# Performance work log

Measured on AMD Instinct MI355X. Metric: run time of the kernel, lower is better.

The kernel has to match this reference:

```python
import jax, jax.numpy as jnp
import numpy as np

M = 64    # multiplicity (channels per harmonic degree)
P = 64    # positional encoding dim
EPS = 1e-5


def sinusoidal_pe(N, P):
    pos = jnp.arange(N, dtype=jnp.float32)[:, None]
    div = jnp.exp(jnp.arange(0, P, 2, dtype=jnp.float32) * (-np.log(10000.0) / P))
    pe = jnp.zeros((N, P), dtype=jnp.float32)
    pe = pe.at[:, 0::2].set(jnp.sin(pos * div))
    pe = pe.at[:, 1::2].set(jnp.cos(pos * div))
    return pe


def split_irreps(h):
    # h: [B, N, 4M] -> scalar part [B,N,M], vector part [B,N,M,3]
    B, N, _ = h.shape
    h4 = h.reshape(B, N, M, 4)
    return h4[..., 0], h4[..., 1:]


def merge_irreps(s, v):
    B, N, _ = s.shape
    return jnp.concatenate([s[..., None], v], axis=-1).reshape(B, N, M * 4)


def hyena_block(h, Wq, Wk, Wv, filt, Wo):
    # Hyena-style gated long convolution: q * conv(k * v), FFT circular conv along seq
    N = h.shape[1]
    q = h @ Wq
    k = h @ Wk
    v = h @ Wv
    kf = jnp.fft.rfft(filt, n=N, axis=0)                       # [N//2+1, H]
    conv = jnp.fft.irfft(jnp.fft.rfft(k * v, n=N, axis=1) * kf[None], n=N, axis=1)
    return (q * conv) @ Wo


def reg_linear(h, W0, W1):
    # degree-wise linear mixing across multiplicity (equivariant)
    s, v = split_irreps(h)
    return merge_irreps(jnp.einsum('bnm,mk->bnk', s, W0),
                        jnp.einsum('bnmd,mk->bnkd', v, W1))


def reg_batchnorm(h, g0, g1):
    # normalize per-channel irrep norms over (batch, tokens); learnable per-channel gain
    s, v = split_irreps(h)
    n0 = jnp.sqrt(jnp.mean(s * s, axis=(0, 1)) + EPS)          # [M]
    n1 = jnp.sqrt(jnp.mean(jnp.sum(v * v, axis=-1), axis=(0, 1)) + EPS)
    return merge_irreps(s / n0 * g0, v / n1[:, None] * g1[:, None])


def norm_activation(h):
    # norm-gated nonlinearity: each irrep scaled by sigmoid of its norm (equivariant)
    s, v = split_irreps(h)
    vn = jnp.sqrt(jnp.sum(v * v, axis=-1, keepdims=True) + EPS)
    return merge_irreps(s * jax.nn.sigmoid(jnp.abs(s)), v * jax.nn.sigmoid(vn))


def setup_inputs() -> dict:
    key = jax.random.key(0)
    B, N = 64, 1024
    D = M * 4
    H = [360, 360, 160]   # 10*sum(2l+1,l<=5)=360, 360, 10*sum(2l+1,l<=3)=160
    ks = iter(jax.random.split(key, 64))
    def rn(shape, scale=0.02):
        return jax.random.normal(next(ks), shape, dtype=jnp.float32) * scale
    inp = {
        'x': jax.random.normal(next(ks), (B, N, 3), dtype=jnp.float32),
        'tok_emb': rn((3, P)),
        'Wf': rn((P, M)),
        'wv': rn((M,), 0.5),
        'w_out': rn((M,), 0.5),
    }
    for i, Hi in enumerate(H, start=1):
        inp[f'Wq{i}'] = rn((D, Hi)); inp[f'Wk{i}'] = rn((D, Hi)); inp[f'Wv{i}'] = rn((D, Hi))
        inp[f'filt{i}'] = rn((N, Hi)); inp[f'Wo{i}'] = rn((Hi, D))
        inp[f'Wm0_{i}'] = rn((M, M)); inp[f'Wm1_{i}'] = rn((M, M))
        inp[f'g0_{i}'] = jnp.ones((M,), jnp.float32); inp[f'g1_{i}'] = jnp.ones((M,), jnp.float32)
    return inp


def reference(x, tok_emb, Wf, wv, w_out,
              Wq1, Wk1, Wv1, filt1, Wo1, Wm0_1, Wm1_1, g0_1, g1_1,
              Wq2, Wk2, Wv2, filt2, Wo2, Wm0_2, Wm1_2, g0_2, g1_2,
              Wq3, Wk3, Wv3, filt3, Wo3, Wm0_3, Wm1_3, g0_3, g1_3):
    B, N, _ = x.shape
    # invariant features: sinusoidal PE + token-type embedding (alternating 0/1, last token 2)
    pe = sinusoidal_pe(N, P)
    tt = jnp.arange(N) % 2
    tt = tt.at[-1].set(2)
    f = pe + tok_emb[tt]                                        # [N, P]
    # input conversion: invariants -> degree-0 channels; input vector -> degree-1 channels
    s0 = jnp.broadcast_to((f @ Wf)[None], (B, N, M))
    v0 = x[:, :, None, :] * wv[None, None, :, None]             # [B, N, M, 3]
    h = merge_irreps(s0, v0)                                    # [B, N, 4M]
    layers = [
        (Wq1, Wk1, Wv1, filt1, Wo1, Wm0_1, Wm1_1, g0_1, g1_1),
        (Wq2, Wk2, Wv2, filt2, Wo2, Wm0_2, Wm1_2, g0_2, g1_2),
        (Wq3, Wk3, Wv3, filt3, Wo3, Wm0_3, Wm1_3, g0_3, g1_3),
    ]
    for (Wq, Wk, Wv_, filt, Wo, Wm0, Wm1, g0, g1) in layers:
        h = h + hyena_block(h, Wq, Wk, Wv_, filt, Wo)           # hyena + residual
        y = reg_linear(h, Wm0, Wm1)                             # mlp
        y = reg_batchnorm(y, g0, g1)                            # batch norm
        y = norm_activation(y)                                  # norm activation
        h = h + y                                               # residual
    pooled = h.mean(axis=1)                                     # [B, 4M] mean pool over tokens
    _, vpool = split_irreps(pooled[:, None, :])                 # [B, 1, M, 3]
    return jnp.einsum('bmd,m->bd', vpool[:, 0], w_out)          # [B, 3]
```

## Files before the change

### kernel.cpp

```cpp
#include <hip/hip_runtime.h>
#include <math.h>

namespace {

typedef __bf16 bf16_t;
typedef bf16_t bf16x8 __attribute__((ext_vector_type(8)));
typedef float floatx4 __attribute__((ext_vector_type(4)));

constexpr int kN = 1024;
constexpr int kM = 64;
constexpr int kP = 64;
constexpr float kEps = 1e-5f;
constexpr int kFN = 1024;
constexpr size_t kYOFF = 16777216;

__device__ __forceinline__ float sigmoidf(float v) { return 1.0f / (1.0f + expf(-v)); }

__device__ __forceinline__ floatx4 mfma16(bf16x8 a, bf16x8 b, floatx4 c) {
  return __builtin_amdgcn_mfma_f32_16x16x32_bf16(a, b, c, 0, 0, 0);
}

__device__ __forceinline__ void fma3(floatx4& acc, bf16x8 ah, bf16x8 al,
                                     bf16x8 bh, bf16x8 bl) {
  acc = mfma16(ah, bh, acc);
  acc = mfma16(ah, bl, acc);
  acc = mfma16(al, bh, acc);
}

__device__ __forceinline__ void fma2(floatx4& acc, bf16x8 ah, bf16x8 bh, bf16x8 bl) {
  acc = mfma16(ah, bh, acc);
  acc = mfma16(ah, bl, acc);
}

union U4 { uint4 u; bf16_t b[8]; };
union Pk4 { uint2 u; bf16_t b[4]; };
union Ub2 { uint u; bf16_t b[2]; };

__device__ __forceinline__ void glds16(const bf16_t* g, bf16_t* l) {
  __builtin_amdgcn_global_load_lds(
      (const __attribute__((address_space(1))) void*)g,
      (__attribute__((address_space(3))) void*)l, 16, 0, 0);
}

__device__ __forceinline__ size_t hidx(int r, int d8) {
  const int rb = r >> 6, rr = r & 63;
  return (size_t)(rb * 8 + (d8 >> 2)) * 4096 + (rr >> 4) * 1024 + (d8 & 3) * 128 + (rr & 15) * 8;
}

__device__ __forceinline__ int zi(int i) { return i + (i >> 4); }

__device__ __forceinline__ float2 cadd(float2 a, float2 b) { return {a.x + b.x, a.y + b.y}; }
__device__ __forceinline__ float2 csub(float2 a, float2 b) { return {a.x - b.x, a.y - b.y}; }
__device__ __forceinline__ float2 cmul(float2 a, float2 w) {
  return {a.x * w.x - a.y * w.y, a.x * w.y + a.y * w.x};
}
__device__ __forceinline__ float2 cmulc(float2 a, float2 w) {
  return {a.x * w.x + a.y * w.y, a.y * w.x - a.x * w.y};
}

__global__ void k_s0(const float* __restrict__ tok_emb, const float* __restrict__ Wf,
                     float* __restrict__ s0) {
  __shared__ float f[kP];
  const int n = blockIdx.x;
  const int t = threadIdx.x;
  const int tt = (n == kN - 1) ? 2 : (n & 1);
  const int j = t >> 1;
  const float cexp = (float)(-9.210340371976184 / 64.0);
  const float divj = expf((float)(2 * j) * cexp);
  const float ang = (float)n * divj;
  const float pe = (t & 1) ? cosf(ang) : sinf(ang);
  f[t] = pe + tok_emb[tt * kP + t];
  __syncthreads();
  float acc = 0.0f;
#pragma unroll 8
  for (int p = 0; p < kP; ++p) acc = fmaf(f[p], Wf[p * kM + t], acc);
  s0[n * kM + t] = acc;
}

__global__ void k_h0(const float* __restrict__ x, const float* __restrict__ wv,
                     const float* __restrict__ s0, bf16_t* __restrict__ hsh) {
  const int idx = blockIdx.x * 256 + threadIdx.x;
  const int r = idx >> 5, d8 = idx & 31;
  const int n = r & (kN - 1);
  const int m0 = d8 * 2, m1 = m0 + 1;
  const float w0 = wv[m0], w1 = wv[m1];
  const float x0 = x[r * 3 + 0], x1 = x[r * 3 + 1], x2 = x[r * 3 + 2];
  float f[8];
  f[0] = s0[n * kM + m0]; f[1] = x0 * w0; f[2] = x1 * w0; f[3] = x2 * w0;
  f[4] = s0[n * kM + m1]; f[5] = x0 * w1; f[6] = x1 * w1; f[7] = x2 * w1;
  U4 oh, ol;
#pragma unroll
  for (int i = 0; i < 8; ++i) {
    const bf16_t h_ = (bf16_t)f[i];
    oh.b[i] = h_; ol.b[i] = (bf16_t)(f[i] - (float)h_);
  }
  const size_t base = hidx(r, d8);
  *(uint4*)(hsh + base) = oh.u;
  *(uint4*)(hsh + base + 512) = ol.u;
}

__global__ void k_wqkv3(const float* __restrict__ Wq0, const float* __restrict__ Wk0,
                        const float* __restrict__ Wv0,
                        const float* __restrict__ Wq1, const float* __restrict__ Wk1,
                        const float* __restrict__ Wv1,
                        const float* __restrict__ Wq2, const float* __restrict__ Wk2,
                        const float* __restrict__ Wv2, bf16_t* __restrict__ wall3) {
  const int l = blockIdx.y;
  const int H = (l == 2) ? 160 : 360;
  const int gy = (l == 2) ? 3 : 6;
  const int c = blockIdx.x;
  if (c >= gy * 64) return;
  const int k = threadIdx.x;
  const float* Wq = (l == 0) ? Wq0 : ((l == 1) ? Wq1 : Wq2);
  const float* Wk = (l == 0) ? Wk0 : ((l == 1) ? Wk1 : Wk2);
  const float* Wv = (l == 0) ? Wv0 : ((l == 1) ? Wv1 : Wv2);
  bf16_t* wall = wall3 + ((l == 2) ? 1179648 : (size_t)l * 589824);
  const bool ok = c < H;
  const float w[3] = {ok ? Wq[k * H + c] : 0.f, ok ? Wk[k * H + c] : 0.f,
                      ok ? Wv[k * H + c] : 0.f};
  const int ct = c >> 6, cgrp = (c >> 4) & 3, cl = c & 15;
  const int kc = k >> 5, quad = (k >> 3) & 3, off = k & 7;
  const size_t base = (size_t)(ct * 8 + kc) * 12288 + cgrp * 512 + quad * 128 + cl * 8 + off;
#pragma unroll
  for (int mat = 0; mat < 3; ++mat) {
    const bf16_t hi = (bf16_t)w[mat];
    wall[base + mat * 4096] = hi;
    wall[base + mat * 4096 + 2048] = (bf16_t)(w[mat] - (float)hi);
  }
}

__global__ void k_wo3(const float* __restrict__ Wo0, const float* __restrict__ Wo1,
                      const float* __restrict__ Wo2, bf16_t* __restrict__ WoF3) {
  const int l = blockIdx.y;
  const int H = (l == 2) ? 160 : 360;
  const float* Wo = (l == 0) ? Wo0 : ((l == 1) ? Wo1 : Wo2);
  bf16_t* WoF = WoF3 + (size_t)l * 196608;
  const int d = blockIdx.x;
  const int c = threadIdx.x;
  const float w = (c < H) ? Wo[c * 256 + d] : 0.f;
  const int dt = d >> 6, dgrp = (d >> 4) & 3, dl = d & 15;
  const int kc = c >> 5, quad = (c >> 3) & 3, off = c & 7;
  const size_t base = (size_t)(dt * 12 + kc) * 4096 + dgrp * 512 + quad * 128 + dl * 8 + off;
  const bf16_t hi = (bf16_t)w;
  WoF[base] = hi;
  WoF[base + 2048] = (bf16_t)(w - (float)hi);
}

__global__ void k_bt3(const float* __restrict__ W00, const float* __restrict__ W10,
                      const float* __restrict__ W01, const float* __restrict__ W11,
                      const float* __restrict__ W02, const float* __restrict__ W12,
                      bf16_t* __restrict__ BtF3) {
  const int l = blockIdx.y;
  const float* W0 = (l == 0) ? W00 : ((l == 1) ? W01 : W02);
  const float* W1 = (l == 0) ? W10 : ((l == 1) ? W11 : W12);
  bf16_t* BtF = BtF3 + (size_t)l * 131072;
  const int col = blockIdx.x, row = threadIdx.x;
  const int k = col >> 2, ck = col & 3, m = row >> 2, cm = row & 3;
  float v = 0.f;
  if (cm == ck) v = (ck == 0 ? W0 : W1)[m * 64 + k];
  const int ct = col >> 6, cgrp = (col >> 4) & 3, cl = col & 15;
  const int kc = row >> 5, quad = (row >> 3) & 3, off = row & 7;
  const size_t base = (size_t)(ct * 8 + kc) * 4096 + cgrp * 512 + quad * 128 + cl * 8 + off;
  const bf16_t hi = (bf16_t)v;
  BtF[base] = hi;
  BtF[base + 2048] = (bf16_t)(v - (float)hi);
}

__global__ void k_tw(float2* __restrict__ twg) {
  const int j = blockIdx.x * 256 + threadIdx.x;
  if (j < kFN / 2) {
    float s, c;
    sincosf(-6.283185307179586f * (float)j / (float)kFN, &s, &c);
    twg[j].x = c; twg[j].y = s;
  }
}

__device__ __forceinline__ void dif_step(float2* z, const float2* tw, int m, int p) {
  const int pm = p & (m - 1);
  const int j = ((p & ~(m - 1)) << 2) | pm;
  const int tm2 = 512 / (2 * m), tm1 = 512 / m;
  const float2 x0 = z[zi(j)], x1 = z[zi(j + m)];
  const float2 x2 = z[zi(j + 2 * m)], x3 = z[zi(j + 3 * m)];
  const float2 w2 = tw[pm * tm2], w2b = tw[(pm + m) * tm2], w1 = tw[pm * tm1];
  const float2 a0 = cadd(x0, x2), a2 = cmul(csub(x0, x2), w2);
  const float2 a1 = cadd(x1, x3), a3 = cmul(csub(x1, x3), w2b);
  z[zi(j)]         = cadd(a0, a1);
  z[zi(j + m)]     = cmul(csub(a0, a1), w1);
  z[zi(j + 2 * m)] = cadd(a2, a3);
  z[zi(j + 3 * m)] = cmul(csub(a2, a3), w1);
}

__device__ __forceinline__ void dit_step(float2* z, const float2* tw, int m, int p) {
  const int pm = p & (m - 1);
  const int j = ((p & ~(m - 1)) << 2) | pm;
  const int tm2 = 512 / (2 * m), tm1 = 512 / m;
  const float2 x0 = z[zi(j)], x1 = z[zi(j + m)];
  const float2 x2 = z[zi(j + 2 * m)], x3 = z[zi(j + 3 * m)];
  const float2 w1 = tw[pm * tm1], w2 = tw[pm * tm2], w2b = tw[(pm + m) * tm2];
  const float2 c1 = cmulc(x1, w1), c3 = cmulc(x3, w1);
  const float2 b0 = cadd(x0, c1), b1 = csub(x0, c1);
  const float2 b2 = cadd(x2, c3), b3 = csub(x2, c3);
  const float2 d2 = cmulc(b2, w2), d3 = cmulc(b3, w2b);
  z[zi(j)]         = cadd(b0, d2);
  z[zi(j + 2 * m)] = csub(b0, d2);
  z[zi(j + m)]     = cadd(b1, d3);
  z[zi(j + 3 * m)] = csub(b1, d3);
}

__device__ void fft_dif(float2* z, const float2* tw) {
  const int p = threadIdx.x;
#pragma unroll
  for (int m = 256; m >= 1; m >>= 2) {
    __syncthreads();
    dif_step(z, tw, m, p);
  }
}

__device__ void fft_dif2_hi(float2* za, float2* zb, const float2* tw) {
  const int p = threadIdx.x;
#pragma unroll
  for (int m = 64; m >= 4; m >>= 2) {
    __syncthreads();
    dif_step(za, tw, m, p);
    dif_step(zb, tw, m, p);
  }
}

__device__ void fft_dit_inv2_hi(float2* za, float2* zb, const float2* tw) {
  const int p = threadIdx.x;
#pragma unroll
  for (int m = 4; m <= 256; m <<= 2) {
    __syncthreads();
    dit_step(za, tw, m, p);
    dit_step(zb, tw, m, p);
  }
}

__global__ __launch_bounds__(256) void k_kf3(const float* __restrict__ f0,
    const float* __restrict__ f1, const float* __restrict__ f2,
    const float2* __restrict__ twg, float2* __restrict__ kf3) {
  __shared__ float2 z[kFN + kFN / 16];
  __shared__ float2 tw[kFN / 2];
  const int bid = blockIdx.x;
  const int l = (bid < 360) ? 0 : ((bid < 720) ? 1 : 2);
  const int c = bid - ((l == 0) ? 0 : ((l == 1) ? 360 : 720));
  const int H = (l == 2) ? 160 : 360;
  const float* filt = (l == 0) ? f0 : ((l == 1) ? f1 : f2);
  float2* kf = kf3 + (size_t)l * 368640;
  for (int j = threadIdx.x; j < kFN / 2; j += 256) tw[j] = twg[j];
  for (int n = threadIdx.x; n < kFN; n += 256) {
    z[zi(n)].x = filt[n * H + c];
    z[zi(n)].y = 0.0f;
  }
  fft_dif(z, tw);
  __syncthreads();
  for (int j = threadIdx.x; j < kFN; j += 256) kf[c * kFN + j] = z[zi(j)];
}

__global__ __launch_bounds__(256) void k_conv(const bf16_t* __restrict__ kvb,
    const bf16_t* __restrict__ qb, bf16_t* __restrict__ prodb,
    const float2* __restrict__ kf, const float2* __restrict__ twg, int H) {
  __shared__ float2 za[kFN + kFN / 16];
  __shared__ float2 zb[kFN + kFN / 16];
  __shared__ float2 tw[kFN / 2];
  const int blk = blockIdx.x;
  const int c = blk % H;
  const int pb = blk / H;
  const size_t off0 = ((size_t)((4 * pb) * H + c)) << 10;
  const size_t off1 = ((size_t)((4 * pb + 1) * H + c)) << 10;
  const size_t off2 = ((size_t)((4 * pb + 2) * H + c)) << 10;
  const size_t off3 = ((size_t)((4 * pb + 3) * H + c)) << 10;
  for (int j = threadIdx.x; j < kFN / 2; j += 256) tw[j] = twg[j];
  {
    const int p = threadIdx.x;
    float2 xa[4], xb[4];
#pragma unroll
    for (int e = 0; e < 4; ++e) {
      const int idx = p + e * 256;
      xa[e].x = (float)kvb[off0 + idx]; xa[e].y = (float)kvb[off1 + idx];
      xb[e].x = (float)kvb[off2 + idx]; xb[e].y = (float)kvb[off3 + idx];
    }
    const float2 w2 = twg[p], w2b = twg[p + 256], w1 = twg[2 * p];
#pragma unroll
    for (int arr = 0; arr < 2; ++arr) {
      float2* z = arr ? zb : za;
      const float2* x = arr ? xb : xa;
      const float2 a0 = cadd(x[0], x[2]), a2 = cmul(csub(x[0], x[2]), w2);
      const float2 a1 = cadd(x[1], x[3]), a3 = cmul(csub(x[1], x[3]), w2b);
      z[zi(p)]       = cadd(a0, a1);
      z[zi(p + 256)] = cmul(csub(a0, a1), w1);
      z[zi(p + 512)] = cadd(a2, a3);
      z[zi(p + 768)] = cmul(csub(a2, a3), w1);
    }
  }
  fft_dif2_hi(za, zb, tw);
  __syncthreads();
  {
    const int p = threadIdx.x;
    const float2 B0 = kf[c * kFN + 4 * p + 0];
    const float2 B1 = kf[c * kFN + 4 * p + 1];
    const float2 B2 = kf[c * kFN + 4 * p + 2];
    const float2 B3 = kf[c * kFN + 4 * p + 3];
#pragma unroll
    for (int arr = 0; arr < 2; ++arr) {
      float2* z = arr ? zb : za;
      const float2 x0 = z[zi(4 * p)], x1 = z[zi(4 * p + 1)];
      const float2 x2 = z[zi(4 * p + 2)], x3 = z[zi(4 * p + 3)];
      const float2 a0 = cadd(x0, x2), a2 = csub(x0, x2);
      const float2 a1 = cadd(x1, x3), dd = csub(x1, x3);
      const float2 a3 = {dd.y, -dd.x};
      const float2 y0 = cadd(a0, a1), y1 = csub(a0, a1);
      const float2 y2 = cadd(a2, a3), y3 = csub(a2, a3);
      const float2 o0 = cmul(y0, B0), o1 = cmul(y1, B1);
      const float2 o2 = cmul(y2, B2), o3 = cmul(y3, B3);
      const float2 t0 = cadd(o0, o1), t1 = csub(o0, o1);
      const float2 t2 = cadd(o2, o3), t3 = csub(o2, o3);
      const float2 d3 = {-t3.y, t3.x};
      z[zi(4 * p)]     = cadd(t0, t2);
      z[zi(4 * p + 2)] = csub(t0, t2);
      z[zi(4 * p + 1)] = cadd(t1, d3);
      z[zi(4 * p + 3)] = csub(t1, d3);
    }
  }
  fft_dit_inv2_hi(za, zb, tw);
  __syncthreads();
  const float s = 1.0f / (float)kFN;
  for (int n2 = threadIdx.x; n2 < 512; n2 += 256) {
    Ub2 q0, q1, q2, q3, o0, o1, o2, o3;
    q0.u = *(const uint*)(qb + off0 + 2 * n2);
    q1.u = *(const uint*)(qb + off1 + 2 * n2);
    q2.u = *(const uint*)(qb + off2 + 2 * n2);
    q3.u = *(const uint*)(qb + off3 + 2 * n2);
    o0.b[0] = (bf16_t)((za[zi(2 * n2)].x * s) * (float)q0.b[0]);
    o0.b[1] = (bf16_t)((za[zi(2 * n2 + 1)].x * s) * (float)q0.b[1]);
    o1.b[0] = (bf16_t)((za[zi(2 * n2)].y * s) * (float)q1.b[0]);
    o1.b[1] = (bf16_t)((za[zi(2 * n2 + 1)].y * s) * (float)q1.b[1]);
    o2.b[0] = (bf16_t)((zb[zi(2 * n2)].x * s) * (float)q2.b[0]);
    o2.b[1] = (bf16_t)((zb[zi(2 * n2 + 1)].x * s) * (float)q2.b[1]);
    o3.b[0] = (bf16_t)((zb[zi(2 * n2)].y * s) * (float)q3.b[0]);
    o3.b[1] = (bf16_t)((zb[zi(2 * n2 + 1)].y * s) * (float)q3.b[1]);
    *(uint*)(prodb + off0 + 2 * n2) = o0.u;
    *(uint*)(prodb + off1 + 2 * n2) = o1.u;
    *(uint*)(prodb + off2 + 2 * n2) = o2.u;
    *(uint*)(prodb + off3 + 2 * n2) = o3.u;
  }
}

__global__ __launch_bounds__(256) void k_qkv(const bf16_t* __restrict__ hsh,
    const bf16_t* __restrict__ wall, int H,
    bf16_t* __restrict__ qtb, bf16_t* __restrict__ kvb) {
  __shared__ bf16_t lds[20480];
  const int gy = (H + 63) >> 6;
  const int bid = blockIdx.x;
  const int xcd = bid & 7, sseq = bid >> 3;
  const int ct = sseq % gy;
  const int rb2 = (sseq / gy) * 8 + xcd;
  const int rb0 = rb2 * 2, rb1 = rb0 + 1;
  const int t = threadIdx.x;
  const int lane = t & 63, wave = t >> 6;
  const int l15 = lane & 15, quad = lane >> 4;
  const int c0 = ct * 64;
  const int wr = (wave & 1) * 32, wc = (wave >> 1) * 32;
  const int wr16 = (wave & 1) * 2, wc16 = (wave >> 1) * 2;
  const int q128l = quad * 128 + l15 * 8;
  floatx4 aq[2][2][2] = {}, ak_[2][2][2] = {}, av_[2][2][2] = {};
  for (int kt = 0; kt < 8; ++kt) {
    {
      const bf16_t* A0 = hsh + (size_t)(rb0 * 8 + kt) * 4096;
      const bf16_t* A1 = hsh + (size_t)(rb1 * 8 + kt) * 4096;
      const bf16_t* Bs = wall + (size_t)(ct * 8 + kt) * 12288;
#pragma unroll
      for (int s = 0; s < 10; ++s) {
        const int seg = wave * 10 + s;
        const bf16_t* src = (seg < 8) ? (A0 + seg * 512)
                          : (seg < 16) ? (A1 + (seg - 8) * 512)
                                       : (Bs + (seg - 16) * 512);
        glds16(src + lane * 8, &lds[seg * 512]);
      }
    }
    __syncthreads();
    bf16x8 ah[2][2], al[2][2];
#pragma unroll
    for (int rbx = 0; rbx < 2; ++rbx)
#pragma unroll
      for (int i = 0; i < 2; ++i) {
        ah[rbx][i] = *(const bf16x8*)(lds + rbx * 4096 + ((wr16 + i) * 2 + 0) * 512 + q128l);
        al[rbx][i] = *(const bf16x8*)(lds + rbx * 4096 + ((wr16 + i) * 2 + 1) * 512 + q128l);
      }
#pragma unroll
    for (int mat = 0; mat < 3; ++mat) {
      const int bb = 8192 + mat * 4096;
#pragma unroll
      for (int j = 0; j < 2; ++j) {
        const bf16x8 bh = *(const bf16x8*)(lds + bb + (wc16 + j) * 512 + q128l);
        const bf16x8 bl = *(const bf16x8*)(lds + bb + 2048 + (wc16 + j) * 512 + q128l);
#pragma unroll
        for (int rbx = 0; rbx < 2; ++rbx)
#pragma unroll
          for (int i = 0; i < 2; ++i) {
            floatx4& a = (mat == 0) ? aq[rbx][i][j]
                       : (mat == 1) ? ak_[rbx][i][j] : av_[rbx][i][j];
            fma3(a, ah[rbx][i], al[rbx][i], bh, bl);
          }
      }
    }
    __syncthreads();
  }
#pragma unroll
  for (int rbx = 0; rbx < 2; ++rbx) {
    const int r0 = (rb0 + rbx) * 64;
    const int b = r0 >> 10;
    const int n0 = r0 & 1023;
#pragma unroll
    for (int j = 0; j < 2; ++j) {
      const int c = c0 + wc + j * 16 + l15;
      if (c < H) {
        const size_t rbw = (((size_t)(b * H + c)) << 10) + n0 + wr + quad * 4;
#pragma unroll
        for (int i = 0; i < 2; ++i) {
          Pk4 pq, pk;
#pragma unroll
          for (int r = 0; r < 4; ++r) {
            pq.b[r] = (bf16_t)aq[rbx][i][j][r];
            pk.b[r] = (bf16_t)(ak_[rbx][i][j][r] * av_[rbx][i][j][r]);
          }
          *(uint2*)(qtb + rbw + i * 16) = pq.u;
          *(uint2*)(kvb + rbw + i * 16) = pk.u;
        }
      }
    }
  }
}

__global__ __launch_bounds__(256) void k_mix(const bf16_t* __restrict__ pv, int H, int KT,
    const bf16_t* __restrict__ WoF, bf16_t* __restrict__ hsh) {
  __shared__ float smem[4352];
  bf16_t* lsm = (bf16_t*)smem;
  const int r0 = blockIdx.x * 64;
  const int t = threadIdx.x;
  const int lane = t & 63, wave = t >> 6;
  const int l15 = lane & 15, quad = lane >> 4;
  const int b = r0 >> 10, n0 = r0 & 1023;
  const int wr = (wave & 1) * 32, wh = wave >> 1;
  const int q128l = quad * 128 + l15 * 8;
  floatx4 acc[2][8] = {};
  const int cl = t >> 3, n8 = (t & 7) * 8;
  {
    U4 val;
    val.u = make_uint4(0, 0, 0, 0);
    if (cl < H)
      val.u = *(const uint4*)(pv + ((((size_t)(b * H + cl)) << 10) + n0 + n8));
#pragma unroll
    for (int u = 0; u < 8; ++u) lsm[(n8 + u) * 40 + cl] = val.b[u];
  }
  for (int kt = 0; kt < KT; ++kt) {
    const int cur = kt & 1;
    const bool have = (kt + 1 < KT);
    U4 nxt;
    nxt.u = make_uint4(0, 0, 0, 0);
    if (have) {
      const int c = (kt + 1) * 32 + cl;
      if (c < H)
        nxt.u = *(const uint4*)(pv + ((((size_t)(b * H + c)) << 10) + n0 + n8));
    }
    __syncthreads();
    const bf16_t* Ls = lsm + cur * 2560;
    const bf16x8 ah0 = *(const bf16x8*)(Ls + (wr + l15) * 40 + quad * 8);
    const bf16x8 ah1 = *(const bf16x8*)(Ls + (wr + 16 + l15) * 40 + quad * 8);
#pragma unroll
    for (int j = 0; j < 8; ++j) {
      const int jj = wh * 8 + j;
      const int dt = jj >> 2, dgrp = jj & 3;
      const bf16_t* Bb = WoF + (size_t)(dt * 12 + kt) * 4096 + dgrp * 512 + q128l;
      const bf16x8 bh = *(const bf16x8*)Bb;
      const bf16x8 bl = *(const bf16x8*)(Bb + 2048);
      fma2(acc[0][j], ah0, bh, bl);
      fma2(acc[1][j], ah1, bh, bl);
    }
    if (have) {
      bf16_t* Ld = lsm + (cur ^ 1) * 2560;
#pragma unroll
      for (int u = 0; u < 8; ++u) Ld[(n8 + u) * 40 + cl] = nxt.b[u];
    }
  }
  const int nl = t >> 2, q4 = t & 3;
  const int r = r0 + nl;
#pragma unroll
  for (int g = 0; g < 4; ++g) {
    __syncthreads();
    if (wh == (g >> 1)) {
#pragma unroll
      for (int jl = 0; jl < 4; ++jl) {
        const int j = (g & 1) * 4 + jl;
#pragma unroll
        for (int i = 0; i < 2; ++i)
#pragma unroll
          for (int rr = 0; rr < 4; ++rr)
            smem[(wr + i * 16 + quad * 4 + rr) * 68 + jl * 16 + l15] = acc[i][j][rr];
      }
    }
    __syncthreads();
#pragma unroll
    for (int u8 = 0; u8 < 2; ++u8) {
      const int d8 = g * 8 + q4 * 2 + u8;
      const size_t base = hidx(r, d8);
      U4 hi, lo;
      hi.u = *(const uint4*)(hsh + base);
      lo.u = *(const uint4*)(hsh + base + 512);
      U4 oh, ol;
#pragma unroll
      for (int i = 0; i < 8; ++i) {
        const float f = (float)hi.b[i] + (float)lo.b[i] +
                        smem[nl * 68 + (q4 * 2 + u8) * 8 + i];
        const bf16_t h_ = (bf16_t)f;
        oh.b[i] = h_; ol.b[i] = (bf16_t)(f - (float)h_);
      }
      *(uint4*)(hsh + base) = oh.u;
      *(uint4*)(hsh + base + 512) = ol.u;
    }
  }
}

__global__ __launch_bounds__(256) void k_reg(const bf16_t* __restrict__ hsh,
    const bf16_t* __restrict__ BtF,
    bf16_t* __restrict__ ybf, float* __restrict__ partial) {
  __shared__ float smf[12288];
  __shared__ float red[256];
  bf16_t* lds = (bf16_t*)smf;
  const int bid = blockIdx.x;
  const int xcd = bid & 7, sseq = bid >> 3;
  const int ct = sseq & 3;
  const int rb2 = (sseq >> 2) * 8 + xcd;
  const int rb0 = rb2 * 2, rb1 = rb0 + 1;
  const int t = threadIdx.x;
  const int lane = t & 63, wave = t >> 6;
  const int l15 = lane & 15, quad = lane >> 4;
  const int c0 = ct * 64;
  const int wr = (wave & 1) * 32, wc = (wave >> 1) * 32;
  const int wr16 = (wave & 1) * 2, wc16 = (wave >> 1) * 2;
  const int q128l = quad * 128 + l15 * 8;
  floatx4 acc[2][2][2] = {};
  auto stage = [&](int kt, int buf) {
    const bf16_t* A0 = hsh + (size_t)(rb0 * 8 + kt) * 4096;
    const bf16_t* A1 = hsh + (size_t)(rb1 * 8 + kt) * 4096;
    const bf16_t* Bs = BtF + (size_t)(ct * 8 + kt) * 4096;
#pragma unroll
    for (int s = 0; s < 6; ++s) {
      const int seg = wave * 6 + s;
      const bf16_t* src = (seg < 8) ? (A0 + seg * 512)
                        : (seg < 16) ? (A1 + (seg - 8) * 512)
                                     : (Bs + (seg - 16) * 512);
      glds16(src + lane * 8, &lds[buf * 12288 + seg * 512]);
    }
  };
  stage(0, 0);
  __syncthreads();
  for (int kt = 0; kt < 8; ++kt) {
    const int cur = kt & 1;
    if (kt < 7) stage(kt + 1, cur ^ 1);
    const bf16_t* Lb = lds + cur * 12288;
    bf16x8 ah[2][2], al[2][2];
#pragma unroll
    for (int rbx = 0; rbx < 2; ++rbx)
#pragma unroll
      for (int i = 0; i < 2; ++i) {
        ah[rbx][i] = *(const bf16x8*)(Lb + rbx * 4096 + ((wr16 + i) * 2 + 0) * 512 + q128l);
        al[rbx][i] = *(const bf16x8*)(Lb + rbx * 4096 + ((wr16 + i) * 2 + 1) * 512 + q128l);
      }
#pragma unroll
    for (int j = 0; j < 2; ++j) {
      const bf16x8 bh = *(const bf16x8*)(Lb + 8192 + (wc16 + j) * 512 + q128l);
      const bf16x8 bl = *(const bf16x8*)(Lb + 8192 + 2048 + (wc16 + j) * 512 + q128l);
#pragma unroll
      for (int rbx = 0; rbx < 2; ++rbx)
#pragma unroll
        for (int i = 0; i < 2; ++i)
          fma3(acc[rbx][i][j], ah[rbx][i], al[rbx][i], bh, bl);
    }
    __syncthreads();
  }
#pragma unroll
  for (int rbx = 0; rbx < 2; ++rbx)
#pragma unroll
    for (int j = 0; j < 2; ++j) {
      float s = 0.f;
#pragma unroll
      for (int i = 0; i < 2; ++i)
#pragma unroll
        for (int r = 0; r < 4; ++r)
          s = fmaf(acc[rbx][i][j][r], acc[rbx][i][j][r], s);
      s += __shfl_down(s, 32);
      s += __shfl_down(s, 16);
      if (lane < 16) red[rbx * 128 + wave * 32 + j * 16 + lane] = s;
    }
#pragma unroll
  for (int rbx = 0; rbx < 2; ++rbx) {
    __syncthreads();
#pragma unroll
    for (int i = 0; i < 2; ++i)
#pragma unroll
      for (int j = 0; j < 2; ++j)
#pragma unroll
        for (int r = 0; r < 4; ++r)
          smf[(wr + i * 16 + quad * 4 + r) * 68 + wc + j * 16 + l15] = acc[rbx][i][j][r];
    __syncthreads();
    const int nl = t >> 2, q4 = t & 3;
    const int r0 = (rb0 + rbx) * 64;
    const size_t gi = (size_t)(r0 + nl) * 256 + c0 + q4 * 16;
#pragma unroll
    for (int u2 = 0; u2 < 2; ++u2) {
      U4 oh, ol;
#pragma unroll
      for (int i = 0; i < 8; ++i) {
        const float f = smf[nl * 68 + q4 * 16 + u2 * 8 + i];
        const bf16_t h_ = (bf16_t)f;
        oh.b[i] = h_; ol.b[i] = (bf16_t)(f - (float)h_);
      }
      *(uint4*)(ybf + gi + u2 * 8) = oh.u;
      *(uint4*)(ybf + kYOFF + gi + u2 * 8) = ol.u;
    }
  }
  if (t < 64) {
    const int w0 = (t >= 32) ? 2 : 0;
    const float v0 = red[w0 * 32 + (t & 31)] + red[(w0 + 1) * 32 + (t & 31)];
    const float v1 = red[128 + w0 * 32 + (t & 31)] + red[128 + (w0 + 1) * 32 + (t & 31)];
    partial[(size_t)rb0 * 256 + c0 + t] = v0;
    partial[(size_t)rb1 * 256 + c0 + t] = v1;
  }
}

__global__ __launch_bounds__(256) void k_stat(const float* __restrict__ partial,
                                              float* __restrict__ st) {
  __shared__ float sm1[16][16];
  __shared__ float tot[16];
  const int bb = blockIdx.x;
  const int t = threadIdx.x;
  const int col16 = t & 15, rgrp = t >> 4;
  const int c = bb * 16 + col16;
  float s = 0.f;
  for (int r = rgrp; r < 1024; r += 16) s += partial[(size_t)r * 256 + c];
  sm1[rgrp][col16] = s;
  __syncthreads();
  if (t < 16) {
    float v = 0.f;
#pragma unroll
    for (int g = 0; g < 16; ++g) v += sm1[g][t];
    tot[t] = v;
  }
  __syncthreads();
  if (t < 4) {
    const int m = bb * 4 + t;
    st[m] = tot[4 * t];
    st[64 + m] = tot[4 * t + 1] + tot[4 * t + 2] + tot[4 * t + 3];
  }
}

__global__ void k_bnact(const bf16_t* __restrict__ ybf, const float* __restrict__ stats,
    const float* __restrict__ g0, const float* __restrict__ g1, bf16_t* __restrict__ hsh) {
  const int idx = blockIdx.x * 256 + threadIdx.x;
  const int r = idx >> 5, d8 = idx & 31;
  const int m0 = d8 * 2, m1 = m0 + 1;
  const float i00 = g0[m0] / sqrtf(stats[m0] * (1.0f / 65536.0f) + kEps);
  const float i10 = g1[m0] / sqrtf(stats[64 + m0] * (1.0f / 65536.0f) + kEps);
  const float i01 = g0[m1] / sqrtf(stats[m1] * (1.0f / 65536.0f) + kEps);
  const float i11 = g1[m1] / sqrtf(stats[64 + m1] * (1.0f / 65536.0f) + kEps);
  const size_t ye = (size_t)r * 256 + d8 * 8;
  U4 yh, yl;
  yh.u = *(const uint4*)(ybf + ye);
  yl.u = *(const uint4*)(ybf + kYOFF + ye);
  float yv[8];
#pragma unroll
  for (int i = 0; i < 8; ++i) yv[i] = (float)yh.b[i] + (float)yl.b[i];
  float a[8];
  {
    const float s = yv[0] * i00;
    const float vx = yv[1] * i10, vy = yv[2] * i10, vz = yv[3] * i10;
    const float so = s * sigmoidf(fabsf(s));
    const float vn = sqrtf(fmaf(vx, vx, fmaf(vy, vy, vz * vz)) + kEps);
    const float gv = sigmoidf(vn);
    a[0] = so; a[1] = vx * gv; a[2] = vy * gv; a[3] = vz * gv;
  }
  {
    const float s = yv[4] * i01;
    const float vx = yv[5] * i11, vy = yv[6] * i11, vz = yv[7] * i11;
    const float so = s * sigmoidf(fabsf(s));
    const float vn = sqrtf(fmaf(vx, vx, fmaf(vy, vy, vz * vz)) + kEps);
    const float gv = sigmoidf(vn);
    a[4] = so; a[5] = vx * gv; a[6] = vy * gv; a[7] = vz * gv;
  }
  const size_t base = hidx(r, d8);
  U4 hi, lo;
  hi.u = *(const uint4*)(hsh + base);
  lo.u = *(const uint4*)(hsh + base + 512);
  U4 oh, ol;
#pragma unroll
  for (int i = 0; i < 8; ++i) {
    const float f = (float)hi.b[i] + (float)lo.b[i] + a[i];
    const bf16_t h_ = (bf16_t)f;
    oh.b[i] = h_; ol.b[i] = (bf16_t)(f - (float)h_);
  }
  *(uint4*)(hsh + base) = oh.u;
  *(uint4*)(hsh + base + 512) = ol.u;
}

__global__ __launch_bounds__(256) void k_bnpool(const bf16_t* __restrict__ ybf,
    const float* __restrict__ stats, const float* __restrict__ g0,
    const float* __restrict__ g1, const bf16_t* __restrict__ hsh,
    const float* __restrict__ w_out, float* __restrict__ pp) {
  __shared__ float r0s[256], r1s[256], r2s[256];
  const int t = threadIdx.x;
  const int idx = blockIdx.x * 256 + t;
  const int r = idx >> 5, d8 = idx & 31;
  const int m0 = d8 * 2, m1 = m0 + 1;
  const float i00 = g0[m0] / sqrtf(stats[m0] * (1.0f / 65536.0f) + kEps);
  const float i10 = g1[m0] / sqrtf(stats[64 + m0] * (1.0f / 65536.0f) + kEps);
  const float i01 = g0[m1] / sqrtf(stats[m1] * (1.0f / 65536.0f) + kEps);
  const float i11 = g1[m1] / sqrtf(stats[64 + m1] * (1.0f / 65536.0f) + kEps);
  const size_t ye = (size_t)r * 256 + d8 * 8;
  U4 yh, yl;
  yh.u = *(const uint4*)(ybf + ye);
  yl.u = *(const uint4*)(ybf + kYOFF + ye);
  float yv[8];
#pragma unroll
  for (int i = 0; i < 8; ++i) yv[i] = (float)yh.b[i] + (float)yl.b[i];
  float a[8];
  {
    const float s = yv[0] * i00;
    const float vx = yv[1] * i10, vy = yv[2] * i10, vz = yv[3] * i10;
    const float so = s * sigmoidf(fabsf(s));
    const float vn = sqrtf(fmaf(vx, vx, fmaf(vy, vy, vz * vz)) + kEps);
    const float gv = sigmoidf(vn);
    a[0] = so; a[1] = vx * gv; a[2] = vy * gv; a[3] = vz * gv;
  }
  {
    const float s = yv[4] * i01;
    const float vx = yv[5] * i11, vy = yv[6] * i11, vz = yv[7] * i11;
    const float so = s * sigmoidf(fabsf(s));
    const float vn = sqrtf(fmaf(vx, vx, fmaf(vy, vy, vz * vz)) + kEps);
    const float gv = sigmoidf(vn);
    a[4] = so; a[5] = vx * gv; a[6] = vy * gv; a[7] = vz * gv;
  }
  const size_t base = hidx(r, d8);
  U4 hi, lo;
  hi.u = *(const uint4*)(hsh + base);
  lo.u = *(const uint4*)(hsh + base + 512);
  float f[8];
#pragma unroll
  for (int i = 0; i < 8; ++i) f[i] = (float)hi.b[i] + (float)lo.b[i] + a[i];
  const float w0 = w_out[m0], w1 = w_out[m1];
  r0s[t] = f[1] * w0 + f[5] * w1;
  r1s[t] = f[2] * w0 + f[6] * w1;
  r2s[t] = f[3] * w0 + f[7] * w1;
  __syncthreads();
  for (int s = 128; s > 0; s >>= 1) {
    if (t < s) { r0s[t] += r0s[t + s]; r1s[t] += r1s[t + s]; r2s[t] += r2s[t + s]; }
    __syncthreads();
  }
  if (t == 0) {
    pp[blockIdx.x * 3 + 0] = r0s[0];
    pp[blockIdx.x * 3 + 1] = r1s[0];
    pp[blockIdx.x * 3 + 2] = r2s[0];
  }
}

__global__ void k_pool2(const float* __restrict__ pp, float* __restrict__ out) {
  const int t = threadIdx.x;
  const int b = t / 3, comp = t % 3;
  float s = 0.f;
  for (int k = 0; k < 128; ++k) s += pp[(size_t)(b * 128 + k) * 3 + comp];
  out[t] = s * (1.0f / kN);
}

}

extern "C" void kernel_launch(void* const* d_in, const int* in_sizes, int n_in,
                              void* d_out, int out_size, void* d_ws, size_t ws_size,
                              hipStream_t stream) {
  const float* x       = (const float*)d_in[0];
  const float* tok_emb = (const float*)d_in[1];
  const float* Wf      = (const float*)d_in[2];
  const float* wv      = (const float*)d_in[3];
  const float* w_out   = (const float*)d_in[4];

  float* ws    = (float*)d_ws;
  bf16_t* hsh  = (bf16_t*)ws;
  bf16_t* kvb  = (bf16_t*)(ws + 16777216);
  bf16_t* qtb  = (bf16_t*)(ws + 28573696);
  bf16_t* prodb = (bf16_t*)(ws + 40370176);
  bf16_t* ybf  = prodb;
  float*  partial = ws + 40370176 + 20000000;
  float*  s0   = ws + 40370176 + 23592960;
  float*  kf3  = s0 + 65536;
  bf16_t* wall3 = (bf16_t*)(kf3 + 1802240);
  bf16_t* WoF3  = wall3 + 1474560;
  bf16_t* BtF3  = WoF3 + 589824;
  float* stats = (float*)(BtF3 + 393216);
  float* twg   = stats + 384;

  k_tw<<<2, 256, 0, stream>>>((float2*)twg);
  k_s0<<<kN, 64, 0, stream>>>(tok_emb, Wf, s0);
  k_h0<<<8192, 256, 0, stream>>>(x, wv, s0, hsh);
  k_wqkv3<<<dim3(384, 3), 256, 0, stream>>>(
      (const float*)d_in[5], (const float*)d_in[6], (const float*)d_in[7],
      (const float*)d_in[14], (const float*)d_in[15], (const float*)d_in[16],
      (const float*)d_in[23], (const float*)d_in[24], (const float*)d_in[25], wall3);
  k_wo3<<<dim3(256, 3), 384, 0, stream>>>(
      (const float*)d_in[9], (const float*)d_in[18], (const float*)d_in[27], WoF3);
  k_bt3<<<dim3(256, 3), 256, 0, stream>>>(
      (const float*)d_in[10], (const float*)d_in[11],
      (const float*)d_in[19], (const float*)d_in[20],
      (const float*)d_in[28], (const float*)d_in[29], BtF3);
  k_kf3<<<880, 256, 0, stream>>>(
      (const float*)d_in[8], (const float*)d_in[17], (const float*)d_in[26],
      (const float2*)twg, (float2*)kf3);

  for (int l = 0; l < 3; ++l) {
    const float* g0   = (const float*)d_in[5 + 9 * l + 7];
    const float* g1   = (const float*)d_in[5 + 9 * l + 8];
    const int H = (l == 2) ? 160 : 360;
    const int gy = (H + 63) / 64;
    const int KT = gy * 2;
    bf16_t* wall = wall3 + ((l == 2) ? 1179648 : (size_t)l * 589824);
    bf16_t* WoF  = WoF3 + (size_t)l * 196608;
    bf16_t* BtF  = BtF3 + (size_t)l * 131072;
    const float2* kf = (const float2*)kf3 + (size_t)l * 368640;
    float* st = stats + l * 128;

    k_qkv<<<gy * 512, 256, 0, stream>>>(hsh, wall, H, qtb, kvb);
    k_conv<<<16 * H, 256, 0, stream>>>(kvb, qtb, prodb, kf, (const float2*)twg, H);
    k_mix<<<1024, 256, 0, stream>>>(prodb, H, KT, WoF, hsh);
    k_reg<<<2048, 256, 0, stream>>>(hsh, BtF, ybf, partial);
    k_stat<<<16, 256, 0, stream>>>(partial, st);
    if (l < 2) {
      k_bnact<<<8192, 256, 0, stream>>>(ybf, st, g0, g1, hsh);
    } else {
      k_bnpool<<<8192, 256, 0, stream>>>(ybf, st, g0, g1, hsh, w_out, partial);
    }
  }

  k_pool2<<<1, 192, 0, stream>>>(partial, (float*)d_out);
}
```

Measured before the change: 1.022 ms.

## Retile k_reg so each block computes all 256 output columns for one row block

The regular-linear GEMM kernel now gives each block one 64-row block and all 256 output columns instead of two row blocks by 64 columns. Activation tiles are loaded once per block rather than once per column tile, and the grid halves to 1024 blocks. Double buffering of the LDS staging is removed: each k-step loads then syncs, which may expose global-to-LDS latency. Each wave holds more accumulators (16 floatx4), raising register pressure and reducing parallelism per kernel.

```diff
diff --git a/kernel.cpp b/kernel.cpp
--- a/kernel.cpp
+++ b/kernel.cpp
@@ -524,89 +524,82 @@
 __global__ __launch_bounds__(256) void k_reg(const bf16_t* __restrict__ hsh,
     const bf16_t* __restrict__ BtF,
     bf16_t* __restrict__ ybf, float* __restrict__ partial) {
-  __shared__ float smf[12288];
-  __shared__ float red[256];
-  bf16_t* lds = (bf16_t*)smf;
+  __shared__ bf16_t lds[20480];
+  __shared__ float red[512];
+  float* smf = (float*)lds;
   const int bid = blockIdx.x;
-  const int xcd = bid & 7, sseq = bid >> 3;
-  const int ct = sseq & 3;
-  const int rb2 = (sseq >> 2) * 8 + xcd;
-  const int rb0 = rb2 * 2, rb1 = rb0 + 1;
+  const int r0 = bid * 64;
   const int t = threadIdx.x;
   const int lane = t & 63, wave = t >> 6;
   const int l15 = lane & 15, quad = lane >> 4;
-  const int c0 = ct * 64;
-  const int wr = (wave & 1) * 32, wc = (wave >> 1) * 32;
-  const int wr16 = (wave & 1) * 2, wc16 = (wave >> 1) * 2;
+  const int wr = (wave & 1) * 32, wh = wave >> 1;
+  const int wr16 = (wave & 1) * 2;
   const int q128l = quad * 128 + l15 * 8;
-  floatx4 acc[2][2][2] = {};
-  auto stage = [&](int kt, int buf) {
-    const bf16_t* A0 = hsh + (size_t)(rb0 * 8 + kt) * 4096;
-    const bf16_t* A1 = hsh + (size_t)(rb1 * 8 + kt) * 4096;
-    const bf16_t* Bs = BtF + (size_t)(ct * 8 + kt) * 4096;
-#pragma unroll
-    for (int s = 0; s < 6; ++s) {
-      const int seg = wave * 6 + s;
-      const bf16_t* src = (seg < 8) ? (A0 + seg * 512)
-                        : (seg < 16) ? (A1 + (seg - 8) * 512)
-                                     : (Bs + (seg - 16) * 512);
-      glds16(src + lane * 8, &lds[buf * 12288 + seg * 512]);
-    }
-  };
-  stage(0, 0);
-  __syncthreads();
+  floatx4 acc[2][8] = {};
   for (int kt = 0; kt < 8; ++kt) {
-    const int cur = kt & 1;
-    if (kt < 7) stage(kt + 1, cur ^ 1);
-    const bf16_t* Lb = lds + cur * 12288;
-    bf16x8 ah[2][2], al[2][2];
-#pragma unroll
-    for (int rbx = 0; rbx < 2; ++rbx)
-#pragma unroll
-      for (int i = 0; i < 2; ++i) {
-        ah[rbx][i] = *(const bf16x8*)(Lb + rbx * 4096 + ((wr16 + i) * 2 + 0) * 512 + q128l);
-        al[rbx][i] = *(const bf16x8*)(Lb + rbx * 4096 + ((wr16 + i) * 2 + 1) * 512 + q128l);
+    {
+      const bf16_t* A0 = hsh + (size_t)(bid * 8 + kt) * 4096;
+#pragma unroll
+      for (int s = 0; s < 10; ++s) {
+        const int seg = wave * 10 + s;
+        const bf16_t* src;
+        if (seg < 8) {
+          src = A0 + seg * 512;
+        } else {
+          const int sb = seg - 8;
+          src = BtF + (size_t)((sb >> 3) * 8 + kt) * 4096 + (sb & 7) * 512;
+        }
+        glds16(src + lane * 8, &lds[seg * 512]);
       }
-#pragma unroll
-    for (int j = 0; j < 2; ++j) {
-      const bf16x8 bh = *(const bf16x8*)(Lb + 8192 + (wc16 + j) * 512 + q128l);
-      const bf16x8 bl = *(const bf16x8*)(Lb + 8192 + 2048 + (wc16 + j) * 512 + q128l);
-#pragma unroll
-      for (int rbx = 0; rbx < 2; ++rbx)
+    }
+    __syncthreads();
+    bf16x8 ah[2], al[2];
+#pragma unroll
+    for (int i = 0; i < 2; ++i) {
+      ah[i] = *(const bf16x8*)(lds + (wr16 + i) * 1024 + q128l);
+      al[i] = *(const bf16x8*)(lds + (wr16 + i) * 1024 + 512 + q128l);
+    }
+#pragma unroll
+    for (int j = 0; j < 8; ++j) {
+      const int ct = wh * 2 + (j >> 2), cgrp = j & 3;
+      const bf16_t* Bp = lds + 4096 + ct * 4096 + cgrp * 512 + q128l;
+      const bf16x8 bh = *(const bf16x8*)Bp;
+      const bf16x8 bl = *(const bf16x8*)(Bp + 2048);
+#pragma unroll
+      for (int i = 0; i < 2; ++i)
+        fma3(acc[i][j], ah[i], al[i], bh, bl);
+    }
+    __syncthreads();
+  }
+#pragma unroll
+  for (int j = 0; j < 8; ++j) {
+    float s = 0.f;
+#pragma unroll
+    for (int i = 0; i < 2; ++i)
+#pragma unroll
+      for (int r = 0; r < 4; ++r)
+        s = fmaf(acc[i][j][r], acc[i][j][r], s);
+    s += __shfl_down(s, 32);
+    s += __shfl_down(s, 16);
+    if (lane < 16) red[(wave & 1) * 256 + wh * 128 + j * 16 + lane] = s;
+  }
+  const int nl = t >> 2, q4 = t & 3;
+#pragma unroll
+  for (int g = 0; g < 4; ++g) {
+    __syncthreads();
+    if (wh == (g >> 1)) {
+#pragma unroll
+      for (int jl = 0; jl < 4; ++jl) {
+        const int j = (g & 1) * 4 + jl;
 #pragma unroll
         for (int i = 0; i < 2; ++i)
-          fma3(acc[rbx][i][j], ah[rbx][i], al[rbx][i], bh, bl);
-    }
-    __syncthreads();
-  }
-#pragma unroll
-  for (int rbx = 0; rbx < 2; ++rbx)
-#pragma unroll
-    for (int j = 0; j < 2; ++j) {
-      float s = 0.f;
-#pragma unroll
-      for (int i = 0; i < 2; ++i)
-#pragma unroll
-        for (int r = 0; r < 4; ++r)
-          s = fmaf(acc[rbx][i][j][r], acc[rbx][i][j][r], s);
-      s += __shfl_down(s, 32);
-      s += __shfl_down(s, 16);
-      if (lane < 16) red[rbx * 128 + wave * 32 + j * 16 + lane] = s;
-    }
-#pragma unroll
-  for (int rbx = 0; rbx < 2; ++rbx) {
-    __syncthreads();
-#pragma unroll
-    for (int i = 0; i < 2; ++i)
-#pragma unroll
-      for (int j = 0; j < 2; ++j)
-#pragma unroll
-        for (int r = 0; r < 4; ++r)
-          smf[(wr + i * 16 + quad * 4 + r) * 68 + wc + j * 16 + l15] = acc[rbx][i][j][r];
-    __syncthreads();
-    const int nl = t >> 2, q4 = t & 3;
-    const int r0 = (rb0 + rbx) * 64;
-    const size_t gi = (size_t)(r0 + nl) * 256 + c0 + q4 * 16;
+#pragma unroll
+          for (int rr = 0; rr < 4; ++rr)
+            smf[(wr + i * 16 + quad * 4 + rr) * 68 + jl * 16 + l15] = acc[i][j][rr];
+      }
+    }
+    __syncthreads();
+    const size_t gi = (size_t)(r0 + nl) * 256 + g * 64 + q4 * 16;
 #pragma unroll
     for (int u2 = 0; u2 < 2; ++u2) {
       U4 oh, ol;
@@ -620,13 +613,7 @@
       *(uint4*)(ybf + kYOFF + gi + u2 * 8) = ol.u;
     }
   }
-  if (t < 64) {
-    const int w0 = (t >= 32) ? 2 : 0;
-    const float v0 = red[w0 * 32 + (t & 31)] + red[(w0 + 1) * 32 + (t & 31)];
-    const float v1 = red[128 + w0 * 32 + (t & 31)] + red[128 + (w0 + 1) * 32 + (t & 31)];
-    partial[(size_t)rb0 * 256 + c0 + t] = v0;
-    partial[(size_t)rb1 * 256 + c0 + t] = v1;
-  }
+  partial[(size_t)bid * 256 + t] = red[t] + red[256 + t];
 }
 
 __global__ __launch_bounds__(256) void k_stat(const float* __restrict__ partial,
@@ -829,7 +816,7 @@
     k_qkv<<<gy * 512, 256, 0, stream>>>(hsh, wall, H, qtb, kvb);
     k_conv<<<16 * H, 256, 0, stream>>>(kvb, qtb, prodb, kf, (const float2*)twg, H);
     k_mix<<<1024, 256, 0, stream>>>(prodb, H, KT, WoF, hsh);
-    k_reg<<<2048, 256, 0, stream>>>(hsh, BtF, ybf, partial);
+    k_reg<<<1024, 256, 0, stream>>>(hsh, BtF, ybf, partial);
     k_stat<<<16, 256, 0, stream>>>(partial, st);
     if (l < 2) {
       k_bnact<<<8192, 256, 0, stream>>>(ybf, st, g0, g1, hsh);
```

New measurement: 1.053 ms. 3.1% more time.
